# Performance work log

Measured on AMD Instinct MI355X. Metric: run time of the kernel, lower is better.

The kernel has to match this reference:

```python
import jax, jax.numpy as jnp
import numpy as np

T, B, NS, NC = 100, 4096, 12, 4
N = NS + NC  # tau dim


def setup_inputs() -> dict:
    key = jax.random.key(0)
    k1, k2, k3, k4, k5 = jax.random.split(key, 5)
    # Symmetric PD quadratic cost C = L L^T / N + I  -> well conditioned
    L = jax.random.normal(k1, (T, B, N, N), dtype=jnp.float32) * 0.1
    C = jnp.einsum('tbij,tbkj->tbik', L, L) + jnp.eye(N, dtype=jnp.float32)
    c = jax.random.normal(k2, (T, B, N), dtype=jnp.float32)
    # Linear dynamics x' = F [x;u] + f, state block near identity for stability
    F = jax.random.normal(k3, (T - 1, B, NS, N), dtype=jnp.float32) * 0.02
    A0 = jnp.concatenate([0.99 * jnp.eye(NS, dtype=jnp.float32),
                          jnp.zeros((NS, NC), jnp.float32)], axis=-1)
    F = F + A0  # broadcast over (T-1, B)
    f = jax.random.normal(k4, (T - 1, B, NS), dtype=jnp.float32) * 0.01
    x_init = jax.random.normal(k5, (B, NS), dtype=jnp.float32)
    return {"x_init": x_init, "C": C, "c": c, "F": F, "f": f}


def _lqr_solve(x_init, C, c, F, f):
    ns = x_init.shape[-1]
    # Pad dynamics to length T (terminal step has no dynamics; V starts at 0
    # so the padded zero F/f contribute nothing).
    Fp = jnp.concatenate([F, jnp.zeros_like(F[:1])], axis=0)  # [T,B,ns,n]
    fp = jnp.concatenate([f, jnp.zeros_like(f[:1])], axis=0)  # [T,B,ns]

    def bwd_step(carry, inp):
        V, v = carry                      # [B,ns,ns], [B,ns]
        Ct, ct, Ft, ft = inp
        # Q = C + F^T V F ; q = c + F^T (V f + v)
        Q = Ct + jnp.einsum('bsi,bst,btj->bij', Ft, V, Ft)
        Vf = jnp.einsum('bst,bt->bs', V, ft) + v
        q = ct + jnp.einsum('bsi,bs->bi', Ft, Vf)
        Qxx, Qxu = Q[:, :ns, :ns], Q[:, :ns, ns:]
        Qux, Quu = Q[:, ns:, :ns], Q[:, ns:, ns:]
        qx, qu = q[:, :ns], q[:, ns:]
        # Joint solve for K = -Quu^{-1} Qux, k = -Quu^{-1} qu
        Kk = -jnp.linalg.solve(Quu, jnp.concatenate([Qux, qu[..., None]], axis=-1))
        K, k = Kk[..., :ns], Kk[..., ns]
        Vn = Qxx + jnp.einsum('bij,bjk->bik', Qxu, K)
        Vn = 0.5 * (Vn + jnp.swapaxes(Vn, -1, -2))
        vn = qx + jnp.einsum('bij,bj->bi', Qxu, k)
        return (Vn, vn), (K, k)

    V0 = jnp.zeros((x_init.shape[0], ns, ns), C.dtype)
    v0 = jnp.zeros((x_init.shape[0], ns), C.dtype)
    _, (Kr, kr) = jax.lax.scan(bwd_step, (V0, v0),
                               (C[::-1], c[::-1], Fp[::-1], fp[::-1]))
    K, k = Kr[::-1], kr[::-1]  # [T,B,nc,ns], [T,B,nc]

    def fwd_step(x, inp):
        Ct, ct, Ft, ft, Kt, kt = inp
        u = jnp.einsum('bij,bj->bi', Kt, x) + kt
        tau = jnp.concatenate([x, u], axis=-1)
        cost = 0.5 * jnp.einsum('bi,bij,bj->b', tau, Ct, tau) \
               + jnp.einsum('bi,bi->b', ct, tau)
        xn = jnp.einsum('bij,bj->bi', Ft, tau) + ft
        return xn, (x, u, cost)

    _, (xs, us, costs) = jax.lax.scan(fwd_step, x_init, (C, c, Fp, fp, K, k))
    return xs, us, jnp.sum(costs, axis=0)


def reference(x_init, C, c, F, f):
    # MPC with QuadCost + LinDx and no box constraints: the iLQR loop
    # converges in one exact LQR solve (Riccati backward + forward rollout).
    x, u, objs = _lqr_solve(x_init, C, c, F, f)
    return x, u, objs
```

## Files before the change

### kernel.cpp

```cpp
#include <hip/hip_runtime.h>
#include <hip/hip_fp16.h>

#define TT 100
#define BB 4096
#define GS 516

#define FENCE() asm volatile("s_waitcnt lgkmcnt(0)" ::: "memory")

__device__ __forceinline__ float pairsum32(float x){
  return x + __shfl_xor(x, 32, 64);
}

template<int CTRL>
__device__ __forceinline__ float ror_add(float x){
  int r = __builtin_amdgcn_update_dpp(0, __float_as_int(x), CTRL, 0xF, 0xF, true);
  return x + __int_as_float(r);
}
__device__ __forceinline__ float reduce16_dpp(float x){
  x = ror_add<0x128>(x);
  x = ror_add<0x124>(x);
  x = ror_add<0x122>(x);
  x = ror_add<0x121>(x);
  return x;
}

template<int KMODE>
__device__ __forceinline__ void storeK(void* wsv, size_t of, int l, float X0,float X1,float X2,float X3){
  if (KMODE==0){
    float* wsb=(float*)wsv + of*52;
    if (l<12)       ((float4*)wsb)[l]  = make_float4(X0,X1,X2,X3);
    else if (l==12) ((float4*)wsb)[12] = make_float4(X0,X1,X2,X3);
  } else {
    __half* wsb=(__half*)wsv + of*52;
    if (l<12){
      wsb[l*4+0]=__float2half(X0); wsb[l*4+1]=__float2half(X1);
      wsb[l*4+2]=__float2half(X2); wsb[l*4+3]=__float2half(X3);
    } else if (l==12){
      wsb[48]=__float2half(X0); wsb[49]=__float2half(X1);
      wsb[50]=__float2half(X2); wsb[51]=__float2half(X3);
    }
  }
}
template<int KMODE>
__device__ __forceinline__ float4 loadKcol(const void* wsv, size_t of, int l){
  if (KMODE==0) return ((const float4*)((const float*)wsv + of*52))[l];
  const __half* p=(const __half*)wsv + of*52 + l*4;
  return make_float4(__half2float(p[0]),__half2float(p[1]),__half2float(p[2]),__half2float(p[3]));
}
template<int KMODE>
__device__ __forceinline__ float loadkk(const void* wsv, size_t of, int r){
  if (KMODE==0) return ((const float*)wsv)[of*52+48+r];
  return __half2float(((const __half*)wsv)[of*52+48+r]);
}

template<int KMODE>
__global__ __launch_bounds__(256)
void lqr_fused(const float* __restrict__ xinit,
               const float* __restrict__ Cg,
               const float* __restrict__ cg,
               const float* __restrict__ Fg,
               const float* __restrict__ fg,
               float* __restrict__ out,
               void* __restrict__ wsv)
{
  __shared__ float smem[GS*8];
  const int tid    = threadIdx.x;
  const int lane   = tid & 63;
  const int l      = lane & 15;
  const int h      = lane >> 5;
  const int w      = (lane >> 4) & 1;
  const int gi     = (tid >> 6)*2 + w;
  const int b      = blockIdx.x*8 + gi;
  const int base16 = lane & 16;

  float* __restrict__ V   = smem + gi*GS;
  float* __restrict__ Fl  = V + 144;
  float* __restrict__ Qxu = V + 384;
  float* __restrict__ Quu = V + 432;
  float* __restrict__ vv  = V + 448;
  float* __restrict__ tb  = V + 460;

  float4 sCa,sCb; float sc_;
  float4 sFa=make_float4(0,0,0,0),sFb=sFa; float sf_=0.f;
  {
    const size_t of = ((size_t)(TT-1)*BB + b);
    const float4* pc = (const float4*)(Cg + of*256 + l*16);
    sCa=pc[2*h]; sCb=pc[2*h+1];
    sc_ = cg[of*16 + l];
  }

  for (int tt=TT-1; tt>=0; --tt){
    const bool hasF = (tt < TT-1);
    float4 Ca=sCa,Cb=sCb; float rc=sc_;
    float4 Fa=sFa,Fb=sFb; float rf=sf_;

    if (hasF && l<12){
      float4* q=(float4*)(Fl + l*20);
      q[2*h]=Fa; q[2*h+1]=Fb;
      if (h==0) tb[l]=rf;
    }
    FENCE();

    if (tt>0){
      const size_t of = ((size_t)(tt-1)*BB + b);
      const float4* pc=(const float4*)(Cg + of*256 + l*16);
      sCa=pc[2*h]; sCb=pc[2*h+1];
      sc_=cg[of*16+l];
      if (l<12){
        const float4* pf=(const float4*)(Fg + of*192 + l*16);
        sFa=pf[2*h]; sFb=pf[2*h+1];
        if (h==0) sf_=fg[of*12+l];
      }
    }

    const float R0=Ca.x,R1=Ca.y,R2=Ca.z,R3=Ca.w,R4=Cb.x,R5=Cb.y,R6=Cb.z,R7v=Cb.w;
    float Qp[16];
    Qp[0]=h?0.f:R0; Qp[1]=h?0.f:R1; Qp[2]=h?0.f:R2; Qp[3]=h?0.f:R3;
    Qp[4]=h?0.f:R4; Qp[5]=h?0.f:R5; Qp[6]=h?0.f:R6; Qp[7]=h?0.f:R7v;
    Qp[8]=h?R0:0.f; Qp[9]=h?R1:0.f; Qp[10]=h?R2:0.f; Qp[11]=h?R3:0.f;
    Qp[12]=h?R4:0.f; Qp[13]=h?R5:0.f; Qp[14]=h?R6:0.f; Qp[15]=h?R7v:0.f;
    float qvp = h? 0.f : rc;

    if (hasF){
      float FtL[6], FtH[6];
      #pragma unroll
      for (int k2=0;k2<6;k2++){ FtL[k2]=Fl[k2*20+l]; FtH[k2]=Fl[(6+k2)*20+l]; }
      const int s0=6*h;
      float Wl[6];
      #pragma unroll
      for (int k2=0;k2<6;k2++){
        const float4* vr=(const float4*)(V+(s0+k2)*12);
        float4 v0=vr[0],v1=vr[1],v2=vr[2];
        Wl[k2]= v0.x*FtL[0]+v0.y*FtL[1]+v0.z*FtL[2]+v0.w*FtL[3]
              + v1.x*FtL[4]+v1.y*FtL[5]+v1.z*FtH[0]+v1.w*FtH[1]
              + v2.x*FtH[2]+v2.y*FtH[3]+v2.z*FtH[4]+v2.w*FtH[5];
      }
      #pragma unroll
      for (int k2=0;k2<6;k2++){
        const float4* fr=(const float4*)(Fl + (s0+k2)*20);
        float4 f0=fr[0],f1=fr[1],f2=fr[2],f3=fr[3];
        float w2=Wl[k2];
        Qp[0]+=f0.x*w2;  Qp[1]+=f0.y*w2;  Qp[2]+=f0.z*w2;  Qp[3]+=f0.w*w2;
        Qp[4]+=f1.x*w2;  Qp[5]+=f1.y*w2;  Qp[6]+=f1.z*w2;  Qp[7]+=f1.w*w2;
        Qp[8]+=f2.x*w2;  Qp[9]+=f2.y*w2;  Qp[10]+=f2.z*w2; Qp[11]+=f2.w*w2;
        Qp[12]+=f3.x*w2; Qp[13]+=f3.y*w2; Qp[14]+=f3.z*w2; Qp[15]+=f3.w*w2;
      }
      const float2* tbp=(const float2*)(tb + s0);
      const float2* vvp=(const float2*)(vv + s0);
      const float2 t0=tbp[0],t1=tbp[1],t2=tbp[2];
      const float2 u0=vvp[0],u1=vvp[1],u2=vvp[2];
      qvp += Wl[0]*t0.x + Wl[1]*t0.y + Wl[2]*t1.x
           + Wl[3]*t1.y + Wl[4]*t2.x + Wl[5]*t2.y;
      const float g0=h?FtH[0]:FtL[0], g1=h?FtH[1]:FtL[1], g2=h?FtH[2]:FtL[2],
                  g3=h?FtH[3]:FtL[3], g4=h?FtH[4]:FtL[4], g5=h?FtH[5]:FtL[5];
      qvp += g0*u0.x + g1*u0.y + g2*u1.x + g3*u1.y + g4*u2.x + g5*u2.y;
    }

    float Qc[16];
    #pragma unroll
    for (int i=0;i<16;i++) Qc[i] = pairsum32(Qp[i]);
    float qv = pairsum32(qvp);

    if (h==0 && l>=12){
      const int cc=l-12;
      ((float4*)Quu)[cc] = make_float4(Qc[12],Qc[13],Qc[14],Qc[15]);
      float4* qx=(float4*)(Qxu + cc*12);
      qx[0]=make_float4(Qc[0],Qc[1],Qc[2],Qc[3]);
      qx[1]=make_float4(Qc[4],Qc[5],Qc[6],Qc[7]);
      qx[2]=make_float4(Qc[8],Qc[9],Qc[10],Qc[11]);
    }
    FENCE();

    float qu0=__shfl(qv,base16+12,64),qu1=__shfl(qv,base16+13,64),
          qu2=__shfl(qv,base16+14,64),qu3=__shfl(qv,base16+15,64);
    float b0,b1,b2,b3;
    if (l<12){b0=-Qc[12];b1=-Qc[13];b2=-Qc[14];b3=-Qc[15];}
    else     {b0=-qu0;b1=-qu1;b2=-qu2;b3=-qu3;}

    const float4 quu0=((const float4*)Quu)[0], quu1=((const float4*)Quu)[1],
                 quu2=((const float4*)Quu)[2], quu3=((const float4*)Quu)[3];
    float a00=quu0.x,a10=quu0.y,a20=quu0.z,a30=quu0.w;
    float a01=quu1.x,a11=quu1.y,a21=quu1.z,a31=quu1.w;
    float a02=quu2.x,a12=quu2.y,a22=quu2.z,a32=quu2.w;
    float a03=quu3.x,a13=quu3.y,a23=quu3.z,a33=quu3.w;

    float i0=1.0f/a00;
    float m10=a10*i0,m20=a20*i0,m30=a30*i0;
    a11-=m10*a01;a12-=m10*a02;a13-=m10*a03;b1-=m10*b0;
    a21-=m20*a01;a22-=m20*a02;a23-=m20*a03;b2-=m20*b0;
    a31-=m30*a01;a32-=m30*a02;a33-=m30*a03;b3-=m30*b0;
    float i1=1.0f/a11;
    float m21=a21*i1,m31=a31*i1;
    a22-=m21*a12;a23-=m21*a13;b2-=m21*b1;
    a32-=m31*a12;a33-=m31*a13;b3-=m31*b1;
    float i2=1.0f/a22;
    float m32=a32*i2;
    a33-=m32*a23;b3-=m32*b2;
    float X3=b3/a33;
    float X2=(b2-a23*X3)*i2;
    float X1=(b1-a12*X2-a13*X3)*i1;
    float X0=(b0-a01*X1-a02*X2-a03*X3)*i0;

    float c0=-qu0,c1=-qu1,c2=-qu2,c3=-qu3;
    c1-=m10*c0; c2-=m20*c0; c3-=m30*c0;
    c2-=m21*c1; c3-=m31*c1;
    c3-=m32*c2;
    const float k3=c3/a33;
    const float k2v=(c2-a23*k3)*i2;
    const float k1=(c1-a12*k2v-a13*k3)*i1;
    const float k0=(c0-a01*k1-a02*k2v-a03*k3)*i0;

    if (h==0) storeK<KMODE>(wsv, (size_t)tt*BB+b, l, X0,X1,X2,X3);

    if (l<12){
      const int i0i=6*h;
      float Vn[6];
      #pragma unroll
      for (int k2=0;k2<6;k2++) Vn[k2] = h? Qc[6+k2] : Qc[k2];
      #pragma unroll
      for (int r=0;r<4;r++){
        const float Xr=(r==0)?X0:(r==1)?X1:(r==2)?X2:X3;
        const float2* qx2=(const float2*)(Qxu + r*12 + i0i);
        float2 x0=qx2[0],x1=qx2[1],x2=qx2[2];
        Vn[0]+=x0.x*Xr; Vn[1]+=x0.y*Xr; Vn[2]+=x1.x*Xr;
        Vn[3]+=x1.y*Xr; Vn[4]+=x2.x*Xr; Vn[5]+=x2.y*Xr;
      }
      float2* vwr=(float2*)(V + l*12 + i0i);
      vwr[0]=make_float2(Vn[0],Vn[1]);
      vwr[1]=make_float2(Vn[2],Vn[3]);
      vwr[2]=make_float2(Vn[4],Vn[5]);
      if (h==0){
        vv[l] = qv + Qc[12]*k0 + Qc[13]*k1 + Qc[14]*k2v + Qc[15]*k3;
      }
    }
  }

  asm volatile("s_waitcnt vmcnt(0)" ::: "memory");

  float xj = (h==0 && l<12)? xinit[(size_t)b*12+l] : 0.f;
  double costacc=0.0;

  float4 sF0=make_float4(0,0,0,0),sF1=sF0,sF2=sF0,sF3=sF0;
  float4 sK=make_float4(0,0,0,0); float sk_=0.f;
  {
    const float4* pc=(const float4*)(Cg + (size_t)b*256 + l*16);
    sCa=pc[2*h]; sCb=pc[2*h+1];
    sc_=cg[(size_t)b*16+l];
    if (h==0 && l<12){
      const float4* pf=(const float4*)(Fg + (size_t)b*192 + l*16);
      sF0=pf[0];sF1=pf[1];sF2=pf[2];sF3=pf[3];
      sf_=fg[(size_t)b*12+l];
      sK=loadKcol<KMODE>(wsv,(size_t)b,l);
    }
    if (h==0 && l>=12) sk_=loadkk<KMODE>(wsv,(size_t)b,l-12);
  }

  for (int t=0;t<TT;t++){
    float4 Ca=sCa,Cb=sCb; float rc=sc_;
    float4 F0=sF0,F1=sF1,F2=sF2,F3=sF3; float rf=sf_;
    float4 K4=sK; float kl=sk_;

    if (t+1<TT){
      const size_t of=((size_t)(t+1)*BB + b);
      const float4* pc=(const float4*)(Cg + of*256 + l*16);
      sCa=pc[2*h]; sCb=pc[2*h+1];
      sc_=cg[of*16+l];
      if (h==0 && l<12){
        sK=loadKcol<KMODE>(wsv,of,l);
        if (t+1<TT-1){
          const float4* pf=(const float4*)(Fg + of*192 + l*16);
          sF0=pf[0];sF1=pf[1];sF2=pf[2];sF3=pf[3];
          sf_=fg[of*12+l];
        }
      }
      if (h==0 && l>=12) sk_=loadkk<KMODE>(wsv,of,l-12);
    }

    float pr0=0.f,pr1=0.f,pr2=0.f,pr3=0.f;
    if (h==0 && l<12){ pr0=K4.x*xj; pr1=K4.y*xj; pr2=K4.z*xj; pr3=K4.w*xj; }
    pr0=reduce16_dpp(pr0); pr1=reduce16_dpp(pr1);
    pr2=reduce16_dpp(pr2); pr3=reduce16_dpp(pr3);

    float* tbuf = tb + (t&1)*16;
    float tauj=0.f;
    if (h==0){
      if (l<12) tauj=xj;
      else {
        const float ur=(l==12)?pr0:(l==13)?pr1:(l==14)?pr2:pr3;
        tauj=ur+kl;
      }
      tbuf[l]=tauj;
    }
    FENCE();

    const float taul = tbuf[l];

    const float4* tp=(const float4*)tbuf;
    const float4 ta=tp[2*h], tb4=tp[2*h+1];

    float dot_p = Ca.x*ta.x + Ca.y*ta.y + Ca.z*ta.z + Ca.w*ta.w
                + Cb.x*tb4.x + Cb.y*tb4.y + Cb.z*tb4.z + Cb.w*tb4.w;
    costacc += (double)( taul*0.5f*dot_p + (h==0 ? taul*rc : 0.f) );

    if (h==0){
      if (l<12) out[(size_t)t*BB*12 + (size_t)b*12 + l] = xj;
      else      out[(size_t)TT*BB*12 + (size_t)t*BB*4 + (size_t)b*4 + (l-12)] = tauj;
    }

    if (t<TT-1 && h==0 && l<12){
      const float4 t0=tp[0],t1=tp[1],t2=tp[2],t3=tp[3];
      xj = rf
         + F0.x*t0.x+F0.y*t0.y+F0.z*t0.z+F0.w*t0.w
         + F1.x*t1.x+F1.y*t1.y+F1.z*t1.z+F1.w*t1.w
         + F2.x*t2.x+F2.y*t2.y+F2.z*t2.z+F2.w*t2.w
         + F3.x*t3.x+F3.y*t3.y+F3.z*t3.z+F3.w*t3.w;
    }
  }

  costacc+=__shfl_xor(costacc,1,64); costacc+=__shfl_xor(costacc,2,64);
  costacc+=__shfl_xor(costacc,4,64); costacc+=__shfl_xor(costacc,8,64);
  costacc+=__shfl_xor(costacc,32,64);
  if (h==0 && l==0) out[(size_t)TT*BB*16 + b]=(float)costacc;
}

extern "C" void kernel_launch(void* const* d_in, const int* in_sizes, int n_in,
                              void* d_out, int out_size, void* d_ws, size_t ws_size,
                              hipStream_t stream){
  (void)in_sizes; (void)n_in; (void)out_size;
  const float* xinit=(const float*)d_in[0];
  const float* C    =(const float*)d_in[1];
  const float* c    =(const float*)d_in[2];
  const float* F    =(const float*)d_in[3];
  const float* f    =(const float*)d_in[4];
  const size_t need_f32 = (size_t)TT*BB*52*sizeof(float);
  if (ws_size >= need_f32){
    lqr_fused<0><<<dim3(BB/8), dim3(256), 0, stream>>>(xinit,C,c,F,f,(float*)d_out,d_ws);
  } else {
    lqr_fused<1><<<dim3(BB/8), dim3(256), 0, stream>>>(xinit,C,c,F,f,(float*)d_out,d_ws);
  }
}
```

Before: 445.2 us.

## Map one batch element per wavefront with quad-lane split and readlane solve

Each batch element now gets a full 64-lane wavefront instead of a half-wave pair, with 4 lanes per row splitting the state reduction. Cross-lane sums use DPP quad reductions, and the Quu matrix and qu are broadcast with readlane rather than going through shared memory. This removes the Qxu/Quu shared staging and one fence per step. In exchange the grid doubles, each wave does less work, and occupancy is bounded via launch_bounds. The forward rollout is remapped onto 16-lane groups with one float4 of C per lane.

```diff
diff --git a/kernel.cpp b/kernel.cpp
--- a/kernel.cpp
+++ b/kernel.cpp
@@ -3,24 +3,29 @@
 
 #define TT 100
 #define BB 4096
-#define GS 516
+#define GS 488
+
 
 #define FENCE() asm volatile("s_waitcnt lgkmcnt(0)" ::: "memory")
 
-__device__ __forceinline__ float pairsum32(float x){
-  return x + __shfl_xor(x, 32, 64);
-}
-
+__device__ __forceinline__ float quadsum(float x){
+  int a = __builtin_amdgcn_update_dpp(0, __float_as_int(x), 0xB1, 0xF, 0xF, true);
+  x += __int_as_float(a);
+  int c = __builtin_amdgcn_update_dpp(0, __float_as_int(x), 0x4E, 0xF, 0xF, true);
+  x += __int_as_float(c);
+  return x;
+}
+__device__ __forceinline__ float readlanef(float x, int srclane){
+  return __int_as_float(__builtin_amdgcn_readlane(__float_as_int(x), srclane));
+}
 template<int CTRL>
 __device__ __forceinline__ float ror_add(float x){
   int r = __builtin_amdgcn_update_dpp(0, __float_as_int(x), CTRL, 0xF, 0xF, true);
   return x + __int_as_float(r);
 }
 __device__ __forceinline__ float reduce16_dpp(float x){
-  x = ror_add<0x128>(x);
-  x = ror_add<0x124>(x);
-  x = ror_add<0x122>(x);
-  x = ror_add<0x121>(x);
+  x = ror_add<0x128>(x); x = ror_add<0x124>(x);
+  x = ror_add<0x122>(x); x = ror_add<0x121>(x);
   return x;
 }
 
@@ -54,7 +59,7 @@
 }
 
 template<int KMODE>
-__global__ __launch_bounds__(256)
+__global__ __launch_bounds__(256,4)
 void lqr_fused(const float* __restrict__ xinit,
                const float* __restrict__ Cg,
                const float* __restrict__ cg,
@@ -63,251 +68,227 @@
                float* __restrict__ out,
                void* __restrict__ wsv)
 {
-  __shared__ float smem[GS*8];
-  const int tid    = threadIdx.x;
-  const int lane   = tid & 63;
-  const int l      = lane & 15;
-  const int h      = lane >> 5;
-  const int w      = (lane >> 4) & 1;
-  const int gi     = (tid >> 6)*2 + w;
-  const int b      = blockIdx.x*8 + gi;
-  const int base16 = lane & 16;
-
-  float* __restrict__ V   = smem + gi*GS;
-  float* __restrict__ Fl  = V + 144;
-  float* __restrict__ Qxu = V + 384;
-  float* __restrict__ Quu = V + 432;
-  float* __restrict__ vv  = V + 448;
-  float* __restrict__ tb  = V + 460;
-
-  float4 sCa,sCb; float sc_;
-  float4 sFa=make_float4(0,0,0,0),sFb=sFa; float sf_=0.f;
+  __shared__ float smem[GS*4];
+  const int tid  = threadIdx.x;
+  const int lane = tid & 63;
+  const int wv   = tid >> 6;
+  const int b    = blockIdx.x*4 + wv;
+  const int l    = lane >> 2;
+  const int qd   = lane & 3;
+
+  float* __restrict__ Vb = smem + wv*GS;
+  float* __restrict__ Fl = Vb + 144;
+  float* __restrict__ vv = Vb + 384;
+  float* __restrict__ tb = Vb + 396;
+
+  if (l<12){
+    const int i0=3*qd;
+    Vb[l*12+i0]=0.f; Vb[l*12+i0+1]=0.f; Vb[l*12+i0+2]=0.f;
+    if (qd==0) vv[l]=0.f;
+  }
+
+  float4 sC0,sC1,sC2,sC3; float sc_;
+  float4 sFst=make_float4(0,0,0,0); float sftv=0.f;
   {
     const size_t of = ((size_t)(TT-1)*BB + b);
-    const float4* pc = (const float4*)(Cg + of*256 + l*16);
-    sCa=pc[2*h]; sCb=pc[2*h+1];
-    sc_ = cg[of*16 + l];
+    const float4* pc=(const float4*)(Cg + of*256 + l*16);
+    sC0=pc[0];sC1=pc[1];sC2=pc[2];sC3=pc[3];
+    sc_=cg[of*16+l];
   }
 
   for (int tt=TT-1; tt>=0; --tt){
     const bool hasF = (tt < TT-1);
-    float4 Ca=sCa,Cb=sCb; float rc=sc_;
-    float4 Fa=sFa,Fb=sFb; float rf=sf_;
-
-    if (hasF && l<12){
-      float4* q=(float4*)(Fl + l*20);
-      q[2*h]=Fa; q[2*h+1]=Fb;
-      if (h==0) tb[l]=rf;
+    float4 C0=sC0,C1=sC1,C2=sC2,C3=sC3; float rc=sc_;
+    float4 Fst=sFst; float ftv=sftv;
+
+    if (hasF){
+      if (lane<48) *(float4*)(Fl + l*20 + 4*qd) = Fst;
+      if (qd==0 && l<12) tb[l]=ftv;
     }
     FENCE();
 
     if (tt>0){
       const size_t of = ((size_t)(tt-1)*BB + b);
       const float4* pc=(const float4*)(Cg + of*256 + l*16);
-      sCa=pc[2*h]; sCb=pc[2*h+1];
+      sC0=pc[0];sC1=pc[1];sC2=pc[2];sC3=pc[3];
       sc_=cg[of*16+l];
-      if (l<12){
-        const float4* pf=(const float4*)(Fg + of*192 + l*16);
-        sFa=pf[2*h]; sFb=pf[2*h+1];
-        if (h==0) sf_=fg[of*12+l];
-      }
-    }
-
-    const float R0=Ca.x,R1=Ca.y,R2=Ca.z,R3=Ca.w,R4=Cb.x,R5=Cb.y,R6=Cb.z,R7v=Cb.w;
-    float Qp[16];
-    Qp[0]=h?0.f:R0; Qp[1]=h?0.f:R1; Qp[2]=h?0.f:R2; Qp[3]=h?0.f:R3;
-    Qp[4]=h?0.f:R4; Qp[5]=h?0.f:R5; Qp[6]=h?0.f:R6; Qp[7]=h?0.f:R7v;
-    Qp[8]=h?R0:0.f; Qp[9]=h?R1:0.f; Qp[10]=h?R2:0.f; Qp[11]=h?R3:0.f;
-    Qp[12]=h?R4:0.f; Qp[13]=h?R5:0.f; Qp[14]=h?R6:0.f; Qp[15]=h?R7v:0.f;
-    float qvp = h? 0.f : rc;
-
+      if (lane<48) sFst = ((const float4*)(Fg + of*192))[lane];
+      if (qd==0 && l<12) sftv = fg[of*12+l];
+    }
+
+    float Qf[16]={0,0,0,0,0,0,0,0,0,0,0,0,0,0,0,0};
+    float qf=0.f;
     if (hasF){
-      float FtL[6], FtH[6];
+      float Ftj[12];
       #pragma unroll
-      for (int k2=0;k2<6;k2++){ FtL[k2]=Fl[k2*20+l]; FtH[k2]=Fl[(6+k2)*20+l]; }
-      const int s0=6*h;
-      float Wl[6];
+      for (int t=0;t<12;t++) Ftj[t]=Fl[t*20+l];
+      const int s0=3*qd;
+      float W[3];
       #pragma unroll
-      for (int k2=0;k2<6;k2++){
-        const float4* vr=(const float4*)(V+(s0+k2)*12);
+      for (int j=0;j<3;j++){
+        const float4* vr=(const float4*)(Vb+(s0+j)*12);
         float4 v0=vr[0],v1=vr[1],v2=vr[2];
-        Wl[k2]= v0.x*FtL[0]+v0.y*FtL[1]+v0.z*FtL[2]+v0.w*FtL[3]
-              + v1.x*FtL[4]+v1.y*FtL[5]+v1.z*FtH[0]+v1.w*FtH[1]
-              + v2.x*FtH[2]+v2.y*FtH[3]+v2.z*FtH[4]+v2.w*FtH[5];
+        W[j]= v0.x*Ftj[0]+v0.y*Ftj[1]+v0.z*Ftj[2]+v0.w*Ftj[3]
+            + v1.x*Ftj[4]+v1.y*Ftj[5]+v1.z*Ftj[6]+v1.w*Ftj[7]
+            + v2.x*Ftj[8]+v2.y*Ftj[9]+v2.z*Ftj[10]+v2.w*Ftj[11];
       }
       #pragma unroll
-      for (int k2=0;k2<6;k2++){
-        const float4* fr=(const float4*)(Fl + (s0+k2)*20);
+      for (int j=0;j<3;j++){
+        const float4* fr=(const float4*)(Fl+(s0+j)*20);
         float4 f0=fr[0],f1=fr[1],f2=fr[2],f3=fr[3];
-        float w2=Wl[k2];
-        Qp[0]+=f0.x*w2;  Qp[1]+=f0.y*w2;  Qp[2]+=f0.z*w2;  Qp[3]+=f0.w*w2;
-        Qp[4]+=f1.x*w2;  Qp[5]+=f1.y*w2;  Qp[6]+=f1.z*w2;  Qp[7]+=f1.w*w2;
-        Qp[8]+=f2.x*w2;  Qp[9]+=f2.y*w2;  Qp[10]+=f2.z*w2; Qp[11]+=f2.w*w2;
-        Qp[12]+=f3.x*w2; Qp[13]+=f3.y*w2; Qp[14]+=f3.z*w2; Qp[15]+=f3.w*w2;
+        const float w=W[j];
+        Qf[0]+=f0.x*w;  Qf[1]+=f0.y*w;  Qf[2]+=f0.z*w;  Qf[3]+=f0.w*w;
+        Qf[4]+=f1.x*w;  Qf[5]+=f1.y*w;  Qf[6]+=f1.z*w;  Qf[7]+=f1.w*w;
+        Qf[8]+=f2.x*w;  Qf[9]+=f2.y*w;  Qf[10]+=f2.z*w; Qf[11]+=f2.w*w;
+        Qf[12]+=f3.x*w; Qf[13]+=f3.y*w; Qf[14]+=f3.z*w; Qf[15]+=f3.w*w;
+        qf += w*tb[s0+j];
       }
-      const float2* tbp=(const float2*)(tb + s0);
-      const float2* vvp=(const float2*)(vv + s0);
-      const float2 t0=tbp[0],t1=tbp[1],t2=tbp[2];
-      const float2 u0=vvp[0],u1=vvp[1],u2=vvp[2];
-      qvp += Wl[0]*t0.x + Wl[1]*t0.y + Wl[2]*t1.x
-           + Wl[3]*t1.y + Wl[4]*t2.x + Wl[5]*t2.y;
-      const float g0=h?FtH[0]:FtL[0], g1=h?FtH[1]:FtL[1], g2=h?FtH[2]:FtL[2],
-                  g3=h?FtH[3]:FtL[3], g4=h?FtH[4]:FtL[4], g5=h?FtH[5]:FtL[5];
-      qvp += g0*u0.x + g1*u0.y + g2*u1.x + g3*u1.y + g4*u2.x + g5*u2.y;
-    }
-
+      const float fta = qd==0?Ftj[0]:qd==1?Ftj[3]:qd==2?Ftj[6]:Ftj[9];
+      const float ftb = qd==0?Ftj[1]:qd==1?Ftj[4]:qd==2?Ftj[7]:Ftj[10];
+      const float ftc = qd==0?Ftj[2]:qd==1?Ftj[5]:qd==2?Ftj[8]:Ftj[11];
+      qf += fta*vv[s0] + ftb*vv[s0+1] + ftc*vv[s0+2];
+    }
+
+    const float Cr[16]={C0.x,C0.y,C0.z,C0.w, C1.x,C1.y,C1.z,C1.w,
+                        C2.x,C2.y,C2.z,C2.w, C3.x,C3.y,C3.z,C3.w};
     float Qc[16];
     #pragma unroll
-    for (int i=0;i<16;i++) Qc[i] = pairsum32(Qp[i]);
-    float qv = pairsum32(qvp);
-
-    if (h==0 && l>=12){
-      const int cc=l-12;
-      ((float4*)Quu)[cc] = make_float4(Qc[12],Qc[13],Qc[14],Qc[15]);
-      float4* qx=(float4*)(Qxu + cc*12);
-      qx[0]=make_float4(Qc[0],Qc[1],Qc[2],Qc[3]);
-      qx[1]=make_float4(Qc[4],Qc[5],Qc[6],Qc[7]);
-      qx[2]=make_float4(Qc[8],Qc[9],Qc[10],Qc[11]);
-    }
-    FENCE();
-
-    float qu0=__shfl(qv,base16+12,64),qu1=__shfl(qv,base16+13,64),
-          qu2=__shfl(qv,base16+14,64),qu3=__shfl(qv,base16+15,64);
-    float b0,b1,b2,b3;
-    if (l<12){b0=-Qc[12];b1=-Qc[13];b2=-Qc[14];b3=-Qc[15];}
-    else     {b0=-qu0;b1=-qu1;b2=-qu2;b3=-qu3;}
-
-    const float4 quu0=((const float4*)Quu)[0], quu1=((const float4*)Quu)[1],
-                 quu2=((const float4*)Quu)[2], quu3=((const float4*)Quu)[3];
-    float a00=quu0.x,a10=quu0.y,a20=quu0.z,a30=quu0.w;
-    float a01=quu1.x,a11=quu1.y,a21=quu1.z,a31=quu1.w;
-    float a02=quu2.x,a12=quu2.y,a22=quu2.z,a32=quu2.w;
-    float a03=quu3.x,a13=quu3.y,a23=quu3.z,a33=quu3.w;
-
-    float i0=1.0f/a00;
-    float m10=a10*i0,m20=a20*i0,m30=a30*i0;
-    a11-=m10*a01;a12-=m10*a02;a13-=m10*a03;b1-=m10*b0;
-    a21-=m20*a01;a22-=m20*a02;a23-=m20*a03;b2-=m20*b0;
-    a31-=m30*a01;a32-=m30*a02;a33-=m30*a03;b3-=m30*b0;
-    float i1=1.0f/a11;
-    float m21=a21*i1,m31=a31*i1;
-    a22-=m21*a12;a23-=m21*a13;b2-=m21*b1;
-    a32-=m31*a12;a33-=m31*a13;b3-=m31*b1;
-    float i2=1.0f/a22;
-    float m32=a32*i2;
-    a33-=m32*a23;b3-=m32*b2;
-    float X3=b3/a33;
-    float X2=(b2-a23*X3)*i2;
-    float X1=(b1-a12*X2-a13*X3)*i1;
-    float X0=(b0-a01*X1-a02*X2-a03*X3)*i0;
-
+    for (int i=0;i<16;i++) Qc[i] = Cr[i] + quadsum(Qf[i]);
+    const float qv = rc + quadsum(qf);
+
+    float a00=readlanef(Qc[12],48),a01=readlanef(Qc[12],52),a02=readlanef(Qc[12],56),a03=readlanef(Qc[12],60);
+    float a10=readlanef(Qc[13],48),a11=readlanef(Qc[13],52),a12=readlanef(Qc[13],56),a13=readlanef(Qc[13],60);
+    float a20=readlanef(Qc[14],48),a21=readlanef(Qc[14],52),a22=readlanef(Qc[14],56),a23=readlanef(Qc[14],60);
+    float a30=readlanef(Qc[15],48),a31=readlanef(Qc[15],52),a32=readlanef(Qc[15],56),a33=readlanef(Qc[15],60);
+    const float qu0=readlanef(qv,48),qu1=readlanef(qv,52),qu2=readlanef(qv,56),qu3=readlanef(qv,60);
+
+    float b0=-Qc[12],b1=-Qc[13],b2=-Qc[14],b3=-Qc[15];
+    const float i0=1.0f/a00;
+    const float m10=a10*i0,m20=a20*i0,m30=a30*i0;
+    a11-=m10*a01;a12-=m10*a02;a13-=m10*a03;
+    a21-=m20*a01;a22-=m20*a02;a23-=m20*a03;
+    a31-=m30*a01;a32-=m30*a02;a33-=m30*a03;
+    b1-=m10*b0;b2-=m20*b0;b3-=m30*b0;
+    const float i1=1.0f/a11;
+    const float m21=a21*i1,m31=a31*i1;
+    a22-=m21*a12;a23-=m21*a13;
+    a32-=m31*a12;a33-=m31*a13;
+    b2-=m21*b1;b3-=m31*b1;
+    const float i2=1.0f/a22;
+    const float m32=a32*i2;
+    a33-=m32*a23;
+    b3-=m32*b2;
+    const float X3=b3/a33;
+    const float X2=(b2-a23*X3)*i2;
+    const float X1=(b1-a12*X2-a13*X3)*i1;
+    const float X0=(b0-a01*X1-a02*X2-a03*X3)*i0;
     float c0=-qu0,c1=-qu1,c2=-qu2,c3=-qu3;
-    c1-=m10*c0; c2-=m20*c0; c3-=m30*c0;
-    c2-=m21*c1; c3-=m31*c1;
+    c1-=m10*c0;c2-=m20*c0;c3-=m30*c0;
+    c2-=m21*c1;c3-=m31*c1;
     c3-=m32*c2;
     const float k3=c3/a33;
     const float k2v=(c2-a23*k3)*i2;
     const float k1=(c1-a12*k2v-a13*k3)*i1;
     const float k0=(c0-a01*k1-a02*k2v-a03*k3)*i0;
 
-    if (h==0) storeK<KMODE>(wsv, (size_t)tt*BB+b, l, X0,X1,X2,X3);
-
+    if (qd==0)
+      storeK<KMODE>(wsv, (size_t)tt*BB+b, l,
+                    l<12?X0:k0, l<12?X1:k1, l<12?X2:k2v, l<12?X3:k3);
+
+    const float base0 = qd==0?Qc[0]:qd==1?Qc[3]:qd==2?Qc[6]:Qc[9];
+    const float base1 = qd==0?Qc[1]:qd==1?Qc[4]:qd==2?Qc[7]:Qc[10];
+    const float base2 = qd==0?Qc[2]:qd==1?Qc[5]:qd==2?Qc[8]:Qc[11];
+    float vn0=base0, vn1=base1, vn2=base2;
+    #pragma unroll
+    for (int r=0;r<4;r++){
+      const float Xr = r==0?X0:r==1?X1:r==2?X2:X3;
+      vn0 += __shfl(base0, 48+4*r+qd, 64) * Xr;
+      vn1 += __shfl(base1, 48+4*r+qd, 64) * Xr;
+      vn2 += __shfl(base2, 48+4*r+qd, 64) * Xr;
+    }
     if (l<12){
-      const int i0i=6*h;
-      float Vn[6];
-      #pragma unroll
-      for (int k2=0;k2<6;k2++) Vn[k2] = h? Qc[6+k2] : Qc[k2];
-      #pragma unroll
-      for (int r=0;r<4;r++){
-        const float Xr=(r==0)?X0:(r==1)?X1:(r==2)?X2:X3;
-        const float2* qx2=(const float2*)(Qxu + r*12 + i0i);
-        float2 x0=qx2[0],x1=qx2[1],x2=qx2[2];
-        Vn[0]+=x0.x*Xr; Vn[1]+=x0.y*Xr; Vn[2]+=x1.x*Xr;
-        Vn[3]+=x1.y*Xr; Vn[4]+=x2.x*Xr; Vn[5]+=x2.y*Xr;
-      }
-      float2* vwr=(float2*)(V + l*12 + i0i);
-      vwr[0]=make_float2(Vn[0],Vn[1]);
-      vwr[1]=make_float2(Vn[2],Vn[3]);
-      vwr[2]=make_float2(Vn[4],Vn[5]);
-      if (h==0){
+      const int i0i=3*qd;
+      Vb[l*12+i0i]=vn0; Vb[l*12+i0i+1]=vn1; Vb[l*12+i0i+2]=vn2;
+      if (qd==0)
         vv[l] = qv + Qc[12]*k0 + Qc[13]*k1 + Qc[14]*k2v + Qc[15]*k3;
-      }
     }
   }
 
   asm volatile("s_waitcnt vmcnt(0)" ::: "memory");
 
-  float xj = (h==0 && l<12)? xinit[(size_t)b*12+l] : 0.f;
+  const int fl = lane & 15;
+  const int g4 = lane >> 4;
+
+  float xj = (g4==0 && fl<12)? xinit[(size_t)b*12+fl] : 0.f;
   double costacc=0.0;
 
-  float4 sF0=make_float4(0,0,0,0),sF1=sF0,sF2=sF0,sF3=sF0;
+  float4 sCa; float sc2_;
+  float4 sF0=make_float4(0,0,0,0),sF1=sF0,sF2=sF0,sF3=sF0; float sf_=0.f;
   float4 sK=make_float4(0,0,0,0); float sk_=0.f;
   {
-    const float4* pc=(const float4*)(Cg + (size_t)b*256 + l*16);
-    sCa=pc[2*h]; sCb=pc[2*h+1];
-    sc_=cg[(size_t)b*16+l];
-    if (h==0 && l<12){
-      const float4* pf=(const float4*)(Fg + (size_t)b*192 + l*16);
+    const float4* pc=(const float4*)(Cg + (size_t)b*256 + fl*16);
+    sCa=pc[g4];
+    sc2_=cg[(size_t)b*16+fl];
+    if (g4==0 && fl<12){
+      const float4* pf=(const float4*)(Fg + (size_t)b*192 + fl*16);
       sF0=pf[0];sF1=pf[1];sF2=pf[2];sF3=pf[3];
-      sf_=fg[(size_t)b*12+l];
-      sK=loadKcol<KMODE>(wsv,(size_t)b,l);
-    }
-    if (h==0 && l>=12) sk_=loadkk<KMODE>(wsv,(size_t)b,l-12);
+      sf_=fg[(size_t)b*12+fl];
+      sK=loadKcol<KMODE>(wsv,(size_t)b,fl);
+    }
+    if (g4==0 && fl>=12) sk_=loadkk<KMODE>(wsv,(size_t)b,fl-12);
   }
 
   for (int t=0;t<TT;t++){
-    float4 Ca=sCa,Cb=sCb; float rc=sc_;
+    float4 Ca=sCa; float rc=sc2_;
     float4 F0=sF0,F1=sF1,F2=sF2,F3=sF3; float rf=sf_;
     float4 K4=sK; float kl=sk_;
 
     if (t+1<TT){
       const size_t of=((size_t)(t+1)*BB + b);
-      const float4* pc=(const float4*)(Cg + of*256 + l*16);
-      sCa=pc[2*h]; sCb=pc[2*h+1];
-      sc_=cg[of*16+l];
-      if (h==0 && l<12){
-        sK=loadKcol<KMODE>(wsv,of,l);
+      const float4* pc=(const float4*)(Cg + of*256 + fl*16);
+      sCa=pc[g4];
+      sc2_=cg[of*16+fl];
+      if (g4==0 && fl<12){
+        sK=loadKcol<KMODE>(wsv,of,fl);
         if (t+1<TT-1){
-          const float4* pf=(const float4*)(Fg + of*192 + l*16);
+          const float4* pf=(const float4*)(Fg + of*192 + fl*16);
           sF0=pf[0];sF1=pf[1];sF2=pf[2];sF3=pf[3];
-          sf_=fg[of*12+l];
+          sf_=fg[of*12+fl];
         }
       }
-      if (h==0 && l>=12) sk_=loadkk<KMODE>(wsv,of,l-12);
+      if (g4==0 && fl>=12) sk_=loadkk<KMODE>(wsv,of,fl-12);
     }
 
     float pr0=0.f,pr1=0.f,pr2=0.f,pr3=0.f;
-    if (h==0 && l<12){ pr0=K4.x*xj; pr1=K4.y*xj; pr2=K4.z*xj; pr3=K4.w*xj; }
+    if (g4==0 && fl<12){ pr0=K4.x*xj; pr1=K4.y*xj; pr2=K4.z*xj; pr3=K4.w*xj; }
     pr0=reduce16_dpp(pr0); pr1=reduce16_dpp(pr1);
     pr2=reduce16_dpp(pr2); pr3=reduce16_dpp(pr3);
 
     float* tbuf = tb + (t&1)*16;
     float tauj=0.f;
-    if (h==0){
-      if (l<12) tauj=xj;
+    if (g4==0){
+      if (fl<12) tauj=xj;
       else {
-        const float ur=(l==12)?pr0:(l==13)?pr1:(l==14)?pr2:pr3;
+        const float ur=(fl==12)?pr0:(fl==13)?pr1:(fl==14)?pr2:pr3;
         tauj=ur+kl;
       }
-      tbuf[l]=tauj;
+      tbuf[fl]=tauj;
     }
     FENCE();
 
-    const float taul = tbuf[l];
-
-    const float4* tp=(const float4*)tbuf;
-    const float4 ta=tp[2*h], tb4=tp[2*h+1];
-
-    float dot_p = Ca.x*ta.x + Ca.y*ta.y + Ca.z*ta.z + Ca.w*ta.w
-                + Cb.x*tb4.x + Cb.y*tb4.y + Cb.z*tb4.z + Cb.w*tb4.w;
-    costacc += (double)( taul*0.5f*dot_p + (h==0 ? taul*rc : 0.f) );
-
-    if (h==0){
-      if (l<12) out[(size_t)t*BB*12 + (size_t)b*12 + l] = xj;
-      else      out[(size_t)TT*BB*12 + (size_t)t*BB*4 + (size_t)b*4 + (l-12)] = tauj;
-    }
-
-    if (t<TT-1 && h==0 && l<12){
+    const float taul = tbuf[fl];
+    const float4 tq = ((const float4*)tbuf)[g4];
+
+    const float dot_p = Ca.x*tq.x + Ca.y*tq.y + Ca.z*tq.z + Ca.w*tq.w;
+    costacc += (double)( taul*0.5f*dot_p + (g4==0 ? taul*rc : 0.f) );
+
+    if (g4==0){
+      if (fl<12) out[(size_t)t*BB*12 + (size_t)b*12 + fl] = xj;
+      else       out[(size_t)TT*BB*12 + (size_t)t*BB*4 + (size_t)b*4 + (fl-12)] = tauj;
+    }
+
+    if (t<TT-1 && g4==0 && fl<12){
+      const float4* tp=(const float4*)tbuf;
       const float4 t0=tp[0],t1=tp[1],t2=tp[2],t3=tp[3];
       xj = rf
          + F0.x*t0.x+F0.y*t0.y+F0.z*t0.z+F0.w*t0.w
@@ -317,10 +298,10 @@
     }
   }
 
-  costacc+=__shfl_xor(costacc,1,64); costacc+=__shfl_xor(costacc,2,64);
-  costacc+=__shfl_xor(costacc,4,64); costacc+=__shfl_xor(costacc,8,64);
-  costacc+=__shfl_xor(costacc,32,64);
-  if (h==0 && l==0) out[(size_t)TT*BB*16 + b]=(float)costacc;
+  costacc+=__shfl_xor(costacc,1,64);  costacc+=__shfl_xor(costacc,2,64);
+  costacc+=__shfl_xor(costacc,4,64);  costacc+=__shfl_xor(costacc,8,64);
+  costacc+=__shfl_xor(costacc,16,64); costacc+=__shfl_xor(costacc,32,64);
+  if (lane==0) out[(size_t)TT*BB*16 + b]=(float)costacc;
 }
 
 extern "C" void kernel_launch(void* const* d_in, const int* in_sizes, int n_in,
@@ -334,8 +315,8 @@
   const float* f    =(const float*)d_in[4];
   const size_t need_f32 = (size_t)TT*BB*52*sizeof(float);
   if (ws_size >= need_f32){
-    lqr_fused<0><<<dim3(BB/8), dim3(256), 0, stream>>>(xinit,C,c,F,f,(float*)d_out,d_ws);
+    lqr_fused<0><<<dim3(BB/4), dim3(256), 0, stream>>>(xinit,C,c,F,f,(float*)d_out,d_ws);
   } else {
-    lqr_fused<1><<<dim3(BB/8), dim3(256), 0, stream>>>(xinit,C,c,F,f,(float*)d_out,d_ws);
-  }
-}
+    lqr_fused<1><<<dim3(BB/4), dim3(256), 0, stream>>>(xinit,C,c,F,f,(float*)d_out,d_ws);
+  }
+}
```

After: 835.5 us. +87.7%, slower.
